# Optimization experiments

Measured on AMD Instinct MI355X. Metric: run time of the kernel, lower is better.

## Reference

```python
import jax, jax.numpy as jnp
import numpy as np

B, S, I, H = 64, 512, 512, 1024

def setup_inputs() -> dict:
    key = jax.random.key(0)
    ks = jax.random.split(key, 6)
    stdv = 1.0 / np.sqrt(H)
    return {
        "inputs": jax.random.normal(ks[0], (B, S, I), dtype=jnp.float32),
        "h0": jax.random.normal(ks[1], (1, B, H), dtype=jnp.float32),
        "weight_ih": jax.random.uniform(ks[2], (3 * H, I), minval=-stdv, maxval=stdv, dtype=jnp.float32),
        "weight_hh": jax.random.uniform(ks[3], (3 * H, H), minval=-stdv, maxval=stdv, dtype=jnp.float32),
        "bias_ih": jax.random.uniform(ks[4], (3 * H,), minval=-stdv, maxval=stdv, dtype=jnp.float32),
        "bias_hh": jax.random.uniform(ks[5], (3 * H,), minval=-stdv, maxval=stdv, dtype=jnp.float32),
    }

def reference(inputs, h0, weight_ih, weight_hh, bias_ih, bias_hh):
    batch, seq, input_size = inputs.shape
    hidden = h0.shape[-1]
    # Split gate weights: order is (r, z, n) as in the torch module's view(3, H, ...)
    whr, whz, whn = weight_hh.reshape(3, hidden, hidden)
    bhr, bhz, bhn = bias_hh.reshape(3, hidden)
    # Precompute all input projections in one big GEMM: [B,S,3H]
    x_gates = jnp.einsum('bsi,gi->bsg', inputs, weight_ih) + bias_ih
    xr, xz, xn = jnp.split(x_gates, 3, axis=-1)
    # time-major for scan: [S,B,H]
    xs = (jnp.swapaxes(xr, 0, 1), jnp.swapaxes(xz, 0, 1), jnp.swapaxes(xn, 0, 1))

    def step(h, x):
        xr_t, xz_t, xn_t = x
        r = jax.nn.sigmoid(xr_t + h @ whr.T + bhr)
        z = jax.nn.sigmoid(xz_t + h @ whz.T + bhz)
        n = jnp.tanh(xn_t + r * (h @ whn.T + bhn))
        h_new = (1.0 - z) * n + z * h
        return h_new, h_new

    hT, outs = jax.lax.scan(step, h0[0], xs)  # outs: [S,B,H]
    outputs = jnp.swapaxes(outs, 0, 1)  # [B,S,H]
    hn = hT[None]  # [1,B,H]
    return outputs, hn
```

## Files before the change

kernel.cpp:

```cpp
#include <hip/hip_runtime.h>


#define B_ 64
#define S_ 512
#define I_ 512
#define H_ 1024

typedef short short8 __attribute__((ext_vector_type(8)));
typedef float f32x4 __attribute__((ext_vector_type(4)));
typedef unsigned long long u64x2 __attribute__((ext_vector_type(2)));

__device__ __forceinline__ unsigned short f2bf(float f) {
    unsigned u = __builtin_bit_cast(unsigned, f);
    u += 0x7fffu + ((u >> 16) & 1u);
    return (unsigned short)(u >> 16);
}
__device__ __forceinline__ float sigm(float x) { return 1.f / (1.f + __expf(-x)); }
__device__ __forceinline__ float tanh_(float x) { return 2.f / (1.f + __expf(-2.f * x)) - 1.f; }

__device__ __forceinline__ f32x4 MFMA(short8 a, short8 b, f32x4 c) {
    return __builtin_amdgcn_mfma_f32_16x16x32_bf16(a, b, c, 0, 0, 0);
}

__device__ __forceinline__ short8 cvt8(float4 a, float4 b) {
    short8 r;
    r[0] = (short)f2bf(a.x); r[1] = (short)f2bf(a.y); r[2] = (short)f2bf(a.z); r[3] = (short)f2bf(a.w);
    r[4] = (short)f2bf(b.x); r[5] = (short)f2bf(b.y); r[6] = (short)f2bf(b.z); r[7] = (short)f2bf(b.w);
    return r;
}
__device__ __forceinline__ short8 load8bf(const float* p) {
    return cvt8(*(const float4*)p, *(const float4*)(p + 4));
}

__launch_bounds__(256, 1)
__global__ void gru_persistent(const float* __restrict__ xin,
                               unsigned short* hbase,
                               unsigned* flags,
                               const float* __restrict__ w_ih,
                               const float* __restrict__ w_hh,
                               const float* __restrict__ b_ihp,
                               const float* __restrict__ b_hhp,
                               const float* __restrict__ h0,
                               float* __restrict__ out) {
    const int tid = threadIdx.x;
    const int w = tid >> 6;
    const int l = tid & 63;
    const int ln = l & 15;
    const int lq = l >> 4;
    const int grp = blockIdx.x & 3;
    const int cu  = blockIdx.x >> 2;
    const int b0 = grp * 16, d0 = cu * 16;

    short8 Whr[8], Whz[8], Whn[8], Wir[4], Wiz[4], Win[4];
    {
        const int nrow = d0 + ln;
        #pragma unroll
        for (int f = 0; f < 8; ++f) {
            int k = w * 256 + f * 32 + lq * 8;
            Whr[f] = load8bf(w_hh + (size_t)(0 * H_ + nrow) * H_ + k);
            Whz[f] = load8bf(w_hh + (size_t)(1 * H_ + nrow) * H_ + k);
            Whn[f] = load8bf(w_hh + (size_t)(2 * H_ + nrow) * H_ + k);
        }
        #pragma unroll
        for (int f = 0; f < 4; ++f) {
            int k = w * 128 + f * 32 + lq * 8;
            Wir[f] = load8bf(w_ih + (size_t)(0 * H_ + nrow) * I_ + k);
            Wiz[f] = load8bf(w_ih + (size_t)(1 * H_ + nrow) * I_ + k);
            Win[f] = load8bf(w_ih + (size_t)(2 * H_ + nrow) * I_ + k);
        }
    }

    const int n_t = tid & 15, m_t = tid >> 4;
    const int d = d0 + n_t;
    const float b_r  = b_ihp[d]          + b_hhp[d];
    const float b_z  = b_ihp[H_ + d]     + b_hhp[H_ + d];
    const float b_in = b_ihp[2 * H_ + d];
    const float b_hn = b_hhp[2 * H_ + d];
    float hprev = h0[(size_t)(b0 + m_t) * H_ + d];

    __shared__ float red[2 * 4 * 4 * 16 * 20];

    const int ha_base = (b0 + ln) * H_ + w * 256 + lq * 8;
    const float* xrow = xin + (size_t)(b0 + ln) * S_ * I_ + w * 128 + lq * 8;

    unsigned* const myflag = flags + grp * 256 + cu * 4 + w;
    unsigned* const pollp  = flags + grp * 256 + w * 64 + l;

    float4 xf[8];
    #pragma unroll
    for (int f = 0; f < 4; ++f) {
        xf[2 * f]     = *(const float4*)(xrow + f * 32);
        xf[2 * f + 1] = *(const float4*)(xrow + f * 32 + 4);
    }

    for (int t = 0; t < S_; ++t) {
        short8 xA[4];
        #pragma unroll
        for (int f = 0; f < 4; ++f) xA[f] = cvt8(xf[2 * f], xf[2 * f + 1]);

        f32x4 ar = {0,0,0,0}, az = {0,0,0,0}, anh = {0,0,0,0}, anx = {0,0,0,0};
        #pragma unroll
        for (int f = 0; f < 4; ++f) {
            ar  = MFMA(xA[f], Wir[f], ar);
            az  = MFMA(xA[f], Wiz[f], az);
            anx = MFMA(xA[f], Win[f], anx);
        }

        short8 hA[8];
        if (t == 0) {
            #pragma unroll
            for (int f = 0; f < 8; ++f)
                hA[f] = load8bf(h0 + (size_t)(b0 + ln) * H_ + w * 256 + f * 32 + lq * 8);
        } else {
            int guard = 0;
            for (;;) {
                unsigned fv = __hip_atomic_load(pollp, __ATOMIC_RELAXED, __HIP_MEMORY_SCOPE_AGENT);
                if (__all((int)(fv >= (unsigned)t))) break;
                if ((++guard & 255) == 0) __builtin_amdgcn_s_sleep(1);
                if (guard > (1 << 20)) break;
            }
            asm volatile("" ::: "memory");
            const unsigned short* hc = hbase + (size_t)(t & 1) * (B_ * H_);
            #pragma unroll
            for (int f = 0; f < 8; ++f) {
                unsigned long long* p = (unsigned long long*)(hc + ha_base + f * 32);
                u64x2 v;
                v[0] = __hip_atomic_load(p,     __ATOMIC_RELAXED, __HIP_MEMORY_SCOPE_AGENT);
                v[1] = __hip_atomic_load(p + 1, __ATOMIC_RELAXED, __HIP_MEMORY_SCOPE_AGENT);
                hA[f] = __builtin_bit_cast(short8, v);
            }
        }

        #pragma unroll
        for (int f = 0; f < 8; ++f) {
            ar  = MFMA(hA[f], Whr[f], ar);
            az  = MFMA(hA[f], Whz[f], az);
            anh = MFMA(hA[f], Whn[f], anh);
        }

        const int pb = (t & 1) ? 5120 : 0;
        {
            int rbase = pb + (w * 16 + ln) * 20 + lq * 4;
            *(f32x4*)&red[rbase]        = ar;
            *(f32x4*)&red[rbase + 1280] = az;
            *(f32x4*)&red[rbase + 2560] = anh;
            *(f32x4*)&red[rbase + 3840] = anx;
        }
        __syncthreads();

        float rp = 0.f, zp = 0.f, nhp = 0.f, nxp = 0.f;
        #pragma unroll
        for (int ww = 0; ww < 4; ++ww) {
            int ib = pb + (ww * 16 + n_t) * 20 + m_t;
            rp  += red[ib];
            zp  += red[ib + 1280];
            nhp += red[ib + 2560];
            nxp += red[ib + 3840];
        }
        float r = sigm(rp + b_r);
        float z = sigm(zp + b_z);
        float nn = tanh_(nxp + b_in + r * (nhp + b_hn));
        float h = nn + z * (hprev - nn);
        hprev = h;

        if (t < S_ - 1) {
            unsigned short* hnx = hbase + (size_t)((t + 1) & 1) * (B_ * H_);
            unsigned hb16 = f2bf(h);
            unsigned ob = (unsigned)__shfl_xor((int)hb16, 1, 64);
            if ((tid & 1) == 0) {
                unsigned packed = (hb16 & 0xffffu) | (ob << 16);
                __hip_atomic_store((unsigned*)(hnx + (size_t)(b0 + m_t) * H_ + d),
                                   packed, __ATOMIC_RELAXED, __HIP_MEMORY_SCOPE_AGENT);
            }
            asm volatile("s_waitcnt vmcnt(0)" ::: "memory");
            if (l == 0)
                __hip_atomic_store(myflag, (unsigned)(t + 1),
                                   __ATOMIC_RELAXED, __HIP_MEMORY_SCOPE_AGENT);
        }

        __builtin_nontemporal_store(h, &out[((size_t)(b0 + m_t) * S_ + t) * H_ + d]);
        if (t == S_ - 1)
            out[(size_t)B_ * S_ * H_ + (size_t)(b0 + m_t) * H_ + d] = h;

        if (t < S_ - 1) {
            const float* xp = xrow + (size_t)(t + 1) * I_;
            #pragma unroll
            for (int f = 0; f < 4; ++f) {
                xf[2 * f]     = *(const float4*)(xp + f * 32);
                xf[2 * f + 1] = *(const float4*)(xp + f * 32 + 4);
            }
        }
    }
}

extern "C" void kernel_launch(void* const* d_in, const int* in_sizes, int n_in,
                              void* d_out, int out_size, void* d_ws, size_t ws_size,
                              hipStream_t stream) {
    const float* xin  = (const float*)d_in[0];
    const float* h0   = (const float*)d_in[1];
    const float* w_ih = (const float*)d_in[2];
    const float* w_hh = (const float*)d_in[3];
    const float* b_ih = (const float*)d_in[4];
    const float* b_hh = (const float*)d_in[5];
    if (n_in >= 4 && in_sizes[2] == 3 * H_ * H_ && in_sizes[3] == 3 * H_ * I_) {
        const float* tmp = w_ih; w_ih = w_hh; w_hh = tmp;
    }
    float* out = (float*)d_out;

    unsigned short* hb = (unsigned short*)d_ws;
    unsigned* flags = (unsigned*)(hb + 2 * (size_t)B_ * H_);

    hipMemsetAsync(flags, 0, 4096, stream);

    hipLaunchKernelGGL(gru_persistent, dim3(256), dim3(256), 0, stream,
                       xin, hb, flags, w_ih, w_hh, b_ih, b_hh, h0, out);
}
```

Before: 2.420 ms.

## Retile GRU blocks to 8 batch rows by 32 hidden units

Each block now owns 8 batch rows and 32 hidden columns instead of 16×16. The block keeps twice as many weight fragments in registers and issues two MFMA column tiles per gate. Each batch group's step barrier now waits on 32 slices (128 flags) instead of 64 CUs, which is meant to cut cross-block synchronisation latency per timestep. The cost is that half of each 16-row MFMA tile is wasted on duplicated batch rows, plus higher register pressure. The poll loop also sleeps more often.

```diff
diff --git a/kernel.cpp b/kernel.cpp
--- a/kernel.cpp
+++ b/kernel.cpp
@@ -8,7 +8,6 @@
 
 typedef short short8 __attribute__((ext_vector_type(8)));
 typedef float f32x4 __attribute__((ext_vector_type(4)));
-typedef unsigned long long u64x2 __attribute__((ext_vector_type(2)));
 
 __device__ __forceinline__ unsigned short f2bf(float f) {
     unsigned u = __builtin_bit_cast(unsigned, f);
@@ -47,30 +46,32 @@
     const int l = tid & 63;
     const int ln = l & 15;
     const int lq = l >> 4;
-    const int grp = blockIdx.x & 3;
-    const int cu  = blockIdx.x >> 2;
-    const int b0 = grp * 16, d0 = cu * 16;
-
-    short8 Whr[8], Whz[8], Whn[8], Wir[4], Wiz[4], Win[4];
-    {
-        const int nrow = d0 + ln;
-        #pragma unroll
-        for (int f = 0; f < 8; ++f) {
-            int k = w * 256 + f * 32 + lq * 8;
-            Whr[f] = load8bf(w_hh + (size_t)(0 * H_ + nrow) * H_ + k);
-            Whz[f] = load8bf(w_hh + (size_t)(1 * H_ + nrow) * H_ + k);
-            Whn[f] = load8bf(w_hh + (size_t)(2 * H_ + nrow) * H_ + k);
-        }
-        #pragma unroll
-        for (int f = 0; f < 4; ++f) {
-            int k = w * 128 + f * 32 + lq * 8;
-            Wir[f] = load8bf(w_ih + (size_t)(0 * H_ + nrow) * I_ + k);
-            Wiz[f] = load8bf(w_ih + (size_t)(1 * H_ + nrow) * I_ + k);
-            Win[f] = load8bf(w_ih + (size_t)(2 * H_ + nrow) * I_ + k);
-        }
-    }
-
-    const int n_t = tid & 15, m_t = tid >> 4;
+    const int grp   = blockIdx.x & 7;
+    const int slice = blockIdx.x >> 3;
+    const int b0 = grp * 8, d0 = slice * 32;
+
+    short8 Whh[3][8][2], Wih[3][4][2];
+    #pragma unroll
+    for (int g = 0; g < 3; ++g) {
+        #pragma unroll
+        for (int kf = 0; kf < 8; ++kf) {
+            #pragma unroll
+            for (int nh = 0; nh < 2; ++nh) {
+                int col = d0 + nh * 16 + ln;
+                Whh[g][kf][nh] = load8bf(w_hh + (size_t)(g * H_ + col) * H_ + w * 256 + kf * 32 + lq * 8);
+            }
+        }
+        #pragma unroll
+        for (int kf = 0; kf < 4; ++kf) {
+            #pragma unroll
+            for (int nh = 0; nh < 2; ++nh) {
+                int col = d0 + nh * 16 + ln;
+                Wih[g][kf][nh] = load8bf(w_ih + (size_t)(g * H_ + col) * I_ + w * 128 + kf * 32 + lq * 8);
+            }
+        }
+    }
+
+    const int n_t = tid & 31, m_t = tid >> 5;
     const int d = d0 + n_t;
     const float b_r  = b_ihp[d]          + b_hhp[d];
     const float b_z  = b_ihp[H_ + d]     + b_hhp[H_ + d];
@@ -78,13 +79,13 @@
     const float b_hn = b_hhp[2 * H_ + d];
     float hprev = h0[(size_t)(b0 + m_t) * H_ + d];
 
-    __shared__ float red[2 * 4 * 4 * 16 * 20];
-
-    const int ha_base = (b0 + ln) * H_ + w * 256 + lq * 8;
-    const float* xrow = xin + (size_t)(b0 + ln) * S_ * I_ + w * 128 + lq * 8;
-
-    unsigned* const myflag = flags + grp * 256 + cu * 4 + w;
-    unsigned* const pollp  = flags + grp * 256 + w * 64 + l;
+    __shared__ float red[2 * 4 * 4 * 32 * 12];
+
+    const int aoff = (b0 + (ln & 7)) * H_ + w * 256 + lq * 8;
+    const float* xrow = xin + (size_t)(b0 + (ln & 7)) * S_ * I_ + w * 128 + lq * 8;
+
+    unsigned* const myflag = flags + grp * 128 + slice * 4 + w;
+    unsigned* const pollp  = flags + grp * 128 + w * 32 + (l & 31);
 
     float4 xf[8];
     #pragma unroll
@@ -98,64 +99,79 @@
         #pragma unroll
         for (int f = 0; f < 4; ++f) xA[f] = cvt8(xf[2 * f], xf[2 * f + 1]);
 
-        f32x4 ar = {0,0,0,0}, az = {0,0,0,0}, anh = {0,0,0,0}, anx = {0,0,0,0};
-        #pragma unroll
-        for (int f = 0; f < 4; ++f) {
-            ar  = MFMA(xA[f], Wir[f], ar);
-            az  = MFMA(xA[f], Wiz[f], az);
-            anx = MFMA(xA[f], Win[f], anx);
+        f32x4 ar[2] = {{0,0,0,0},{0,0,0,0}}, az[2] = {{0,0,0,0},{0,0,0,0}};
+        f32x4 anh[2] = {{0,0,0,0},{0,0,0,0}}, anx[2] = {{0,0,0,0},{0,0,0,0}};
+        #pragma unroll
+        for (int kf = 0; kf < 4; ++kf) {
+            #pragma unroll
+            for (int nh = 0; nh < 2; ++nh) {
+                ar[nh]  = MFMA(xA[kf], Wih[0][kf][nh], ar[nh]);
+                az[nh]  = MFMA(xA[kf], Wih[1][kf][nh], az[nh]);
+                anx[nh] = MFMA(xA[kf], Wih[2][kf][nh], anx[nh]);
+            }
         }
 
         short8 hA[8];
         if (t == 0) {
             #pragma unroll
-            for (int f = 0; f < 8; ++f)
-                hA[f] = load8bf(h0 + (size_t)(b0 + ln) * H_ + w * 256 + f * 32 + lq * 8);
+            for (int kf = 0; kf < 8; ++kf)
+                hA[kf] = load8bf(h0 + (size_t)(b0 + (ln & 7)) * H_ + w * 256 + kf * 32 + lq * 8);
         } else {
             int guard = 0;
             for (;;) {
                 unsigned fv = __hip_atomic_load(pollp, __ATOMIC_RELAXED, __HIP_MEMORY_SCOPE_AGENT);
                 if (__all((int)(fv >= (unsigned)t))) break;
-                if ((++guard & 255) == 0) __builtin_amdgcn_s_sleep(1);
+                if ((++guard & 63) == 0) __builtin_amdgcn_s_sleep(1);
                 if (guard > (1 << 20)) break;
             }
             asm volatile("" ::: "memory");
             const unsigned short* hc = hbase + (size_t)(t & 1) * (B_ * H_);
             #pragma unroll
-            for (int f = 0; f < 8; ++f) {
-                unsigned long long* p = (unsigned long long*)(hc + ha_base + f * 32);
-                u64x2 v;
-                v[0] = __hip_atomic_load(p,     __ATOMIC_RELAXED, __HIP_MEMORY_SCOPE_AGENT);
-                v[1] = __hip_atomic_load(p + 1, __ATOMIC_RELAXED, __HIP_MEMORY_SCOPE_AGENT);
-                hA[f] = __builtin_bit_cast(short8, v);
-            }
-        }
-
-        #pragma unroll
-        for (int f = 0; f < 8; ++f) {
-            ar  = MFMA(hA[f], Whr[f], ar);
-            az  = MFMA(hA[f], Whz[f], az);
-            anh = MFMA(hA[f], Whn[f], anh);
-        }
-
-        const int pb = (t & 1) ? 5120 : 0;
-        {
-            int rbase = pb + (w * 16 + ln) * 20 + lq * 4;
-            *(f32x4*)&red[rbase]        = ar;
-            *(f32x4*)&red[rbase + 1280] = az;
-            *(f32x4*)&red[rbase + 2560] = anh;
-            *(f32x4*)&red[rbase + 3840] = anx;
+            for (int kf = 0; kf < 8; ++kf) {
+                unsigned long long* p = (unsigned long long*)(hc + aoff + kf * 32);
+                unsigned long long v0 = __hip_atomic_load(p,     __ATOMIC_RELAXED, __HIP_MEMORY_SCOPE_AGENT);
+                unsigned long long v1 = __hip_atomic_load(p + 1, __ATOMIC_RELAXED, __HIP_MEMORY_SCOPE_AGENT);
+                unsigned q[4];
+                q[0] = (unsigned)v0; q[1] = (unsigned)(v0 >> 32);
+                q[2] = (unsigned)v1; q[3] = (unsigned)(v1 >> 32);
+                hA[kf] = __builtin_bit_cast(short8, *(ulong2*)q);
+            }
+        }
+
+        #pragma unroll
+        for (int kf = 0; kf < 8; ++kf) {
+            #pragma unroll
+            for (int nh = 0; nh < 2; ++nh) {
+                ar[nh]  = MFMA(hA[kf], Whh[0][kf][nh], ar[nh]);
+                az[nh]  = MFMA(hA[kf], Whh[1][kf][nh], az[nh]);
+                anh[nh] = MFMA(hA[kf], Whh[2][kf][nh], anh[nh]);
+            }
+        }
+
+        const int par = t & 1;
+        if (lq < 2) {
+            #pragma unroll
+            for (int nh = 0; nh < 2; ++nh) {
+                int nidx = nh * 16 + ln;
+                int base0 = (((par * 4 + 0) * 4 + w) * 32 + nidx) * 12 + lq * 4;
+                int base1 = (((par * 4 + 1) * 4 + w) * 32 + nidx) * 12 + lq * 4;
+                int base2 = (((par * 4 + 2) * 4 + w) * 32 + nidx) * 12 + lq * 4;
+                int base3 = (((par * 4 + 3) * 4 + w) * 32 + nidx) * 12 + lq * 4;
+                *(f32x4*)&red[base0] = ar[nh];
+                *(f32x4*)&red[base1] = az[nh];
+                *(f32x4*)&red[base2] = anh[nh];
+                *(f32x4*)&red[base3] = anx[nh];
+            }
         }
         __syncthreads();
 
         float rp = 0.f, zp = 0.f, nhp = 0.f, nxp = 0.f;
         #pragma unroll
         for (int ww = 0; ww < 4; ++ww) {
-            int ib = pb + (ww * 16 + n_t) * 20 + m_t;
-            rp  += red[ib];
-            zp  += red[ib + 1280];
-            nhp += red[ib + 2560];
-            nxp += red[ib + 3840];
+            rp  += red[(((par * 4 + 0) * 4 + ww) * 32 + n_t) * 12 + m_t];
+            zp  += red[(((par * 4 + 1) * 4 + ww) * 32 + n_t) * 12 + m_t];
+            nhp += red[(((par * 4 + 2) * 4 + ww) * 32 + n_t) * 12 + m_t];
+            nxp += red[(((par * 4 + 3) * 4 + ww) * 32 + n_t) * 12 + m_t];
         }
         float r = sigm(rp + b_r);
         float z = sigm(zp + b_z);
@@ -206,11 +222,12 @@
         const float* tmp = w_ih; w_ih = w_hh; w_hh = tmp;
     }
     float* out = (float*)d_out;
+    (void)ws_size;
 
     unsigned short* hb = (unsigned short*)d_ws;
     unsigned* flags = (unsigned*)(hb + 2 * (size_t)B_ * H_);
 
-    hipMemsetAsync(flags, 0, 4096, stream);
+    hipMemsetAsync(flags, 0, 1024 * sizeof(unsigned), stream);
 
     hipLaunchKernelGGL(gru_persistent, dim3(256), dim3(256), 0, stream,
                        xin, hb, flags, w_ih, w_hh, b_ih, b_hh, h0, out);
```

After: 2.658 ms. 9.8% more time.

## Fuse step tags into hidden-state words to drop separate flag polling

Applied to the files above, without the earlier changes.

Each hidden-state element is now stored as a 32-bit word that packs the bf16 value with a 16-bit timestep tag. Consumers poll the data words themselves until every tag matches the expected step, then extract the bf16 halves with a byte permute. This removes the separate flag store, the vmcnt wait before it, the flag poll and the second dependent load round trip per step, along with the per-launch memset. In exchange the hidden-state traffic doubles in bytes, and correctness relies on stale workspace tags never matching the expected step.

```diff
diff --git a/kernel.cpp b/kernel.cpp
--- a/kernel.cpp
+++ b/kernel.cpp
@@ -8,7 +8,7 @@
 
 typedef short short8 __attribute__((ext_vector_type(8)));
 typedef float f32x4 __attribute__((ext_vector_type(4)));
-typedef unsigned long long u64x2 __attribute__((ext_vector_type(2)));
+typedef unsigned uint4_ __attribute__((ext_vector_type(4)));
 
 __device__ __forceinline__ unsigned short f2bf(float f) {
     unsigned u = __builtin_bit_cast(unsigned, f);
@@ -34,8 +34,7 @@
 
 __launch_bounds__(256, 1)
 __global__ void gru_persistent(const float* __restrict__ xin,
-                               unsigned short* hbase,
-                               unsigned* flags,
+                               unsigned* htag,
                                const float* __restrict__ w_ih,
                                const float* __restrict__ w_hh,
                                const float* __restrict__ b_ihp,
@@ -80,11 +79,9 @@
 
     __shared__ float red[2 * 4 * 4 * 16 * 20];
 
-    const int ha_base = (b0 + ln) * H_ + w * 256 + lq * 8;
+    const int hoff = (b0 + ln) * H_ + w * 256 + lq * 8;
     const float* xrow = xin + (size_t)(b0 + ln) * S_ * I_ + w * 128 + lq * 8;
-
-    unsigned* const myflag = flags + grp * 256 + cu * 4 + w;
-    unsigned* const pollp  = flags + grp * 256 + w * 64 + l;
+    unsigned* const hout = htag  + (size_t)(b0 + m_t) * H_ + d;
 
     float4 xf[8];
     #pragma unroll
@@ -112,22 +109,33 @@
             for (int f = 0; f < 8; ++f)
                 hA[f] = load8bf(h0 + (size_t)(b0 + ln) * H_ + w * 256 + f * 32 + lq * 8);
         } else {
+            const unsigned long long* p =
+                (const unsigned long long*)(htag + (size_t)(t & 1) * (B_ * H_) + hoff);
+            const unsigned long long MASKT  = 0x0000ffff0000ffffULL;
+            const unsigned long long expect = (unsigned long long)(unsigned)t * 0x0000000100000001ULL;
+            unsigned long long v[32];
             int guard = 0;
             for (;;) {
-                unsigned fv = __hip_atomic_load(pollp, __ATOMIC_RELAXED, __HIP_MEMORY_SCOPE_AGENT);
-                if (__all((int)(fv >= (unsigned)t))) break;
-                if ((++guard & 255) == 0) __builtin_amdgcn_s_sleep(1);
-                if (guard > (1 << 20)) break;
+                #pragma unroll
+                for (int q = 0; q < 32; ++q)
+                    v[q] = __hip_atomic_load(p + (q >> 2) * 16 + (q & 3),
+                                             __ATOMIC_RELAXED, __HIP_MEMORY_SCOPE_AGENT);
+                unsigned long long diff = 0;
+                #pragma unroll
+                for (int q = 0; q < 32; ++q) diff |= (v[q] ^ expect) & MASKT;
+                if (__all((int)(diff == 0ULL))) break;
+                if ((++guard & 127) == 0) __builtin_amdgcn_s_sleep(1);
+                if (guard > (1 << 18)) break;
             }
-            asm volatile("" ::: "memory");
-            const unsigned short* hc = hbase + (size_t)(t & 1) * (B_ * H_);
             #pragma unroll
-            for (int f = 0; f < 8; ++f) {
-                unsigned long long* p = (unsigned long long*)(hc + ha_base + f * 32);
-                u64x2 v;
-                v[0] = __hip_atomic_load(p,     __ATOMIC_RELAXED, __HIP_MEMORY_SCOPE_AGENT);
-                v[1] = __hip_atomic_load(p + 1, __ATOMIC_RELAXED, __HIP_MEMORY_SCOPE_AGENT);
-                hA[f] = __builtin_bit_cast(short8, v);
+            for (int kf = 0; kf < 8; ++kf) {
+                uint4_ o;
+                #pragma unroll
+                for (int k = 0; k < 4; ++k) {
+                    unsigned long long vv = v[kf * 4 + k];
+                    o[k] = __builtin_amdgcn_perm((unsigned)(vv >> 32), (unsigned)vv, 0x07060302u);
+                }
+                hA[kf] = __builtin_bit_cast(short8, o);
             }
         }
 
@@ -164,18 +172,9 @@
         hprev = h;
 
         if (t < S_ - 1) {
-            unsigned short* hnx = hbase + (size_t)((t + 1) & 1) * (B_ * H_);
-            unsigned hb16 = f2bf(h);
-            unsigned ob = (unsigned)__shfl_xor((int)hb16, 1, 64);
-            if ((tid & 1) == 0) {
-                unsigned packed = (hb16 & 0xffffu) | (ob << 16);
-                __hip_atomic_store((unsigned*)(hnx + (size_t)(b0 + m_t) * H_ + d),
-                                   packed, __ATOMIC_RELAXED, __HIP_MEMORY_SCOPE_AGENT);
-            }
-            asm volatile("s_waitcnt vmcnt(0)" ::: "memory");
-            if (l == 0)
-                __hip_atomic_store(myflag, (unsigned)(t + 1),
-                                   __ATOMIC_RELAXED, __HIP_MEMORY_SCOPE_AGENT);
+            unsigned word = ((unsigned)f2bf(h) << 16) | (unsigned)(t + 1);
+            __hip_atomic_store(hout + (size_t)((t + 1) & 1) * (B_ * H_),
+                               word, __ATOMIC_RELAXED, __HIP_MEMORY_SCOPE_AGENT);
         }
 
         __builtin_nontemporal_store(h, &out[((size_t)(b0 + m_t) * S_ + t) * H_ + d]);
@@ -206,12 +205,10 @@
         const float* tmp = w_ih; w_ih = w_hh; w_hh = tmp;
     }
     float* out = (float*)d_out;
-
-    unsigned short* hb = (unsigned short*)d_ws;
-    unsigned* flags = (unsigned*)(hb + 2 * (size_t)B_ * H_);
-
-    hipMemsetAsync(flags, 0, 4096, stream);
+    (void)ws_size;
+
+    unsigned* htag = (unsigned*)d_ws;
 
     hipLaunchKernelGGL(gru_persistent, dim3(256), dim3(256), 0, stream,
-                       xin, hb, flags, w_ih, w_hh, b_ih, b_hh, h0, out);
-}
+                       xin, htag, w_ih, w_hh, b_ih, b_hh, h0, out);
+}
```

Result: slower. 3.021 ms (+24.9%).
